# Performance work log

Measured on AMD Instinct MI355X. Metric: run time of the kernel, lower is better.

The kernel has to match this reference:

```python
import jax, jax.numpy as jnp
import numpy as np

K = 16  # hardcoded knn count in Density_loss.forward


def _knn_dist(x, k):
    """Squared pairwise distances [B,N,N], then k smallest per point -> [B,N,k]."""
    sq = jnp.sum(x * x, axis=-1)  # [B,N]
    # d[b,i,j] = |xi|^2 + |xj|^2 - 2 xi.xj
    d = sq[:, :, None] + sq[:, None, :] - 2.0 * jnp.einsum('bic,bjc->bij', x, x)
    neg_topk, _ = jax.lax.top_k(-d, k)  # k smallest distances
    return -neg_topk  # [B,N,k]


def setup_inputs() -> dict:
    key = jax.random.key(0)
    k1, k2 = jax.random.split(key)
    seed = jax.random.normal(k1, (8, 2048, 3), dtype=jnp.float32)
    gt_s = jax.random.normal(k2, (8, 2048, 3), dtype=jnp.float32)
    return {"seed": seed, "gt_s": gt_s}


def reference(seed, gt_s):
    seed_dis = _knn_dist(seed, K).mean(axis=-1)  # [B,N]
    gt_dis = _knn_dist(gt_s, K).mean(axis=-1)    # [B,N]
    # dis_avg=True branch: average over points -> [B], then MSE
    dis = seed_dis.mean(axis=-1)
    gt = gt_dis.mean(axis=-1)
    return jnp.mean((dis - gt) ** 2)
```

## Files before the change

### kernel.cpp

```cpp
#include <hip/hip_runtime.h>
#include <math.h>


#define NPTS 2048
#define KSEL 16
#define WAVES_PER_BLOCK 8
#define BLOCK (WAVES_PER_BLOCK * 64)
#define PTS_PER_BLOCK (WAVES_PER_BLOCK * 2)
#define NGROUPS (NPTS / PTS_PER_BLOCK)
#define NBLOCKS (2 * 8 * NGROUPS)

__device__ __forceinline__ int mbcnt64(unsigned long long m) {
  return __builtin_amdgcn_mbcnt_hi(
      (unsigned)(m >> 32), __builtin_amdgcn_mbcnt_lo((unsigned)m, 0u));
}

template <int CTRL, int ROW_MASK>
__device__ __forceinline__ float dpp_add(float v) {
  const int t = __builtin_amdgcn_update_dpp(0, __float_as_int(v), CTRL,
                                            ROW_MASK, 0xf, true);
  return v + __int_as_float(t);
}

__device__ __forceinline__ float wave_sum_dpp(float v) {
  v = dpp_add<0x111, 0xf>(v);
  v = dpp_add<0x112, 0xf>(v);
  v = dpp_add<0x114, 0xf>(v);
  v = dpp_add<0x118, 0xf>(v);
  v = dpp_add<0x142, 0xa>(v);
  v = dpp_add<0x143, 0xc>(v);
  return __int_as_float(__builtin_amdgcn_readlane(__float_as_int(v), 63));
}

__device__ __forceinline__ float dist2(float px, float py, float pz,
                                       float cx, float cy, float cz) {
  float dx = px - cx, dy = py - cy, dz = pz - cz;
  return fmaf(dz, dz, fmaf(dy, dy, dx * dx));
}

__device__ __forceinline__ void gather_candidates(
    const float (&gm)[8], float thr, float px, float py, float pz, int lane,
    const float* xs, const float* ys, const float* zs, int* scrI, bool& ok,
    float& d0, float& d1, float& d2, float& d3) {
  unsigned qmask = 0u;
  int qg = 0;
  #pragma unroll
  for (int m = 0; m < 8; ++m) {
    const bool q = gm[m] <= thr;
    qmask |= q ? (1u << m) : 0u;
    qg += q ? 1 : 0;
  }
  const unsigned long long b0 = __ballot((qg & 1) != 0);
  const unsigned long long b1 = __ballot((qg & 2) != 0);
  const unsigned long long b2 = __ballot((qg & 4) != 0);
  const unsigned long long b3 = __ballot((qg & 8) != 0);
  const int pre =
      mbcnt64(b0) + 2 * mbcnt64(b1) + 4 * mbcnt64(b2) + 8 * mbcnt64(b3);
  const int tot = __popcll(b0) + 2 * __popcll(b1) + 4 * __popcll(b2) +
                  8 * __popcll(b3);
  ok = (tot <= 64);
  if (ok) {
    int pos = pre;
    unsigned mrem = qmask;
    #pragma unroll
    for (int k = 0; k < 2; ++k) {
      const bool w = (mrem != 0u);
      const int m = __ffs(mrem) - 1;
      if (w) scrI[pos] = (lane << 3) | m;
      pos += w ? 1 : 0;
      mrem = w ? (mrem & (mrem - 1u)) : 0u;
    }
    if (__ballot(mrem != 0u) != 0ull) {
      #pragma unroll
      for (int k = 0; k < 6; ++k) {
        const bool w = (mrem != 0u);
        const int m = __ffs(mrem) - 1;
        if (w) scrI[pos] = (lane << 3) | m;
        pos += w ? 1 : 0;
        mrem = w ? (mrem & (mrem - 1u)) : 0u;
      }
    }
  }
  d0 = INFINITY; d1 = INFINITY; d2 = INFINITY; d3 = INFINITY;
  if (ok && lane < tot) {
    const int id = scrI[lane];
    const int o = ((id >> 3) << 2) + ((id & 7) << 8);
    const float4 cx4 = *(const float4*)&xs[o];
    const float4 cy4 = *(const float4*)&ys[o];
    const float4 cz4 = *(const float4*)&zs[o];
    d0 = dist2(px, py, pz, cx4.x, cy4.x, cz4.x);
    d1 = dist2(px, py, pz, cx4.y, cy4.y, cz4.y);
    d2 = dist2(px, py, pz, cx4.z, cy4.z, cz4.z);
    d3 = dist2(px, py, pz, cx4.w, cy4.w, cz4.w);
  }
}

__device__ float fallback_sum16(float px, float py, float pz, int lane,
                                const float* xs, const float* ys,
                                const float* zs) {
  float s = 0.f;
  unsigned consumed = 0u;
  #pragma unroll 1
  for (int r = 0; r < KSEL; ++r) {
    float bv = INFINITY;
    int bi = 0;
    #pragma unroll
    for (int m = 0; m < 8; ++m) {
      const int o = (lane << 2) + (m << 8);
      const float4 cx4 = *(const float4*)&xs[o];
      const float4 cy4 = *(const float4*)&ys[o];
      const float4 cz4 = *(const float4*)&zs[o];
      float dd;
      bool okb;
      dd = dist2(px, py, pz, cx4.x, cy4.x, cz4.x);
      okb = (((consumed >> ((m << 2) + 0)) & 1u) == 0u) && (dd < bv);
      bv = okb ? dd : bv; bi = okb ? ((m << 2) + 0) : bi;
      dd = dist2(px, py, pz, cx4.y, cy4.y, cz4.y);
      okb = (((consumed >> ((m << 2) + 1)) & 1u) == 0u) && (dd < bv);
      bv = okb ? dd : bv; bi = okb ? ((m << 2) + 1) : bi;
      dd = dist2(px, py, pz, cx4.z, cy4.z, cz4.z);
      okb = (((consumed >> ((m << 2) + 2)) & 1u) == 0u) && (dd < bv);
      bv = okb ? dd : bv; bi = okb ? ((m << 2) + 2) : bi;
      dd = dist2(px, py, pz, cx4.w, cy4.w, cz4.w);
      okb = (((consumed >> ((m << 2) + 3)) & 1u) == 0u) && (dd < bv);
      bv = okb ? dd : bv; bi = okb ? ((m << 2) + 3) : bi;
    }
    int bl = lane;
    #pragma unroll
    for (int ofs = 32; ofs >= 1; ofs >>= 1) {
      float ov = __shfl_xor(bv, ofs);
      int ol = __shfl_xor(bl, ofs);
      bool take = (ov < bv) || (ov == bv && ol < bl);
      bv = take ? ov : bv;
      bl = take ? ol : bl;
    }
    s += bv;
    if (lane == bl) consumed |= (1u << bi);
  }
  return s;
}

__global__ __launch_bounds__(BLOCK) void knn_sum16_kernel(
    const float* __restrict__ seed, const float* __restrict__ gt,
    float* __restrict__ out_part) {
  __shared__ float xs[NPTS];
  __shared__ float ys[NPTS];
  __shared__ float zs[NPTS];
  __shared__ int scrI[WAVES_PER_BLOCK][2][64];
  __shared__ float bsums[WAVES_PER_BLOCK];

  const int bid = blockIdx.x;
  const int t = bid >> 10;
  const int b = (bid >> 7) & 7;
  const int g = bid & 127;
  const float* base = (t == 0 ? seed : gt) + b * NPTS * 3;

  const int tid = threadIdx.x;

  {
    const float4* src = (const float4*)base;
    float4 f0 = src[3 * tid + 0];
    float4 f1 = src[3 * tid + 1];
    float4 f2 = src[3 * tid + 2];
    *(float4*)&xs[4 * tid] = make_float4(f0.x, f0.w, f1.z, f2.y);
    *(float4*)&ys[4 * tid] = make_float4(f0.y, f1.x, f1.w, f2.z);
    *(float4*)&zs[4 * tid] = make_float4(f0.z, f1.y, f2.x, f2.w);
  }
  __syncthreads();

  const int wave = tid >> 6;
  const int lane = tid & 63;
  const int iA = g * PTS_PER_BLOCK + wave * 2;
  const int iB = iA + 1;
  const float pax = xs[iA], pay = ys[iA], paz = zs[iA];
  const float pbx = xs[iB], pby = ys[iB], pbz = zs[iB];

  float gmA[8], gmB[8];
  #pragma unroll
  for (int m = 0; m < 8; ++m) {
    const int o = (lane << 2) + (m << 8);
    const float4 cx4 = *(const float4*)&xs[o];
    const float4 cy4 = *(const float4*)&ys[o];
    const float4 cz4 = *(const float4*)&zs[o];
    float a0 = dist2(pax, pay, paz, cx4.x, cy4.x, cz4.x);
    float a1 = dist2(pax, pay, paz, cx4.y, cy4.y, cz4.y);
    float a2 = dist2(pax, pay, paz, cx4.z, cy4.z, cz4.z);
    float a3 = dist2(pax, pay, paz, cx4.w, cy4.w, cz4.w);
    gmA[m] = fminf(fminf(a0, a1), fminf(a2, a3));
    float b0 = dist2(pbx, pby, pbz, cx4.x, cy4.x, cz4.x);
    float b1 = dist2(pbx, pby, pbz, cx4.y, cy4.y, cz4.y);
    float b2 = dist2(pbx, pby, pbz, cx4.z, cy4.z, cz4.z);
    float b3 = dist2(pbx, pby, pbz, cx4.w, cy4.w, cz4.w);
    gmB[m] = fminf(fminf(b0, b1), fminf(b2, b3));
  }
  float lminA = gmA[0], lminB = gmB[0];
  #pragma unroll
  for (int m = 1; m < 8; ++m) {
    lminA = fminf(lminA, gmA[m]);
    lminB = fminf(lminB, gmB[m]);
  }

  const unsigned uA = __float_as_uint(lminA);
  const unsigned uB = __float_as_uint(lminB);
  unsigned loA = 0u, hiA = 0x7F800000u, loB = 0u, hiB = 0x7F800000u;
  bool thA = false, thB = false;
  #pragma unroll 1
  for (int r = 0; r < 16; ++r) {
    if (thA && thB) break;
    const unsigned midA = (loA + hiA) >> 1;
    const unsigned midB = (loB + hiB) >> 1;
    const int cA = __popcll(__ballot(uA <= midA));
    const int cB = __popcll(__ballot(uB <= midB));
    if (!thA) {
      const bool gA = cA >= KSEL;
      hiA = gA ? midA : hiA;
      loA = gA ? loA : midA;
      thA = (cA >= KSEL) && (cA <= 24);
    }
    if (!thB) {
      const bool gB = cB >= KSEL;
      hiB = gB ? midB : hiB;
      loB = gB ? loB : midB;
      thB = (cB >= KSEL) && (cB <= 24);
    }
  }
  const float thrA = __uint_as_float(hiA);
  const float thrB = __uint_as_float(hiB);

  bool okA, okB;
  float a0, a1, a2, a3, b0, b1, b2, b3;
  gather_candidates(gmA, thrA, pax, pay, paz, lane, xs, ys, zs,
                    &scrI[wave][0][0], okA, a0, a1, a2, a3);
  gather_candidates(gmB, thrB, pbx, pby, pbz, lane, xs, ys, zs,
                    &scrI[wave][1][0], okB, b0, b1, b2, b3);

  const unsigned wa0 = __float_as_uint(a0) + 1u, wa1 = __float_as_uint(a1) + 1u;
  const unsigned wa2 = __float_as_uint(a2) + 1u, wa3 = __float_as_uint(a3) + 1u;
  const unsigned wb0 = __float_as_uint(b0) + 1u, wb1 = __float_as_uint(b1) + 1u;
  const unsigned wb2 = __float_as_uint(b2) + 1u, wb3 = __float_as_uint(b3) + 1u;
  unsigned eloA = 0u, ehiA = 0x7F800001u, eloB = 0u, ehiB = 0x7F800001u;
  bool hA = false, hB = false;
  unsigned sA = 0u, sB = 0u;
  #pragma unroll 1
  for (int r = 0; r < 32; ++r) {
    const bool needA = okA && !hA;
    const bool needB = okB && !hB;
    if (!(needA || needB)) break;
    const unsigned midA = (eloA + ehiA) >> 1;
    const unsigned midB = (eloB + ehiB) >> 1;
    const int cA = __popcll(__ballot(wa0 <= midA)) +
                   __popcll(__ballot(wa1 <= midA)) +
                   __popcll(__ballot(wa2 <= midA)) +
                   __popcll(__ballot(wa3 <= midA));
    const int cB = __popcll(__ballot(wb0 <= midB)) +
                   __popcll(__ballot(wb1 <= midB)) +
                   __popcll(__ballot(wb2 <= midB)) +
                   __popcll(__ballot(wb3 <= midB));
    if (needA) {
      if (cA >= KSEL) ehiA = midA; else eloA = midA;
      if (cA == KSEL) { hA = true; sA = midA; }
    }
    if (needB) {
      if (cB >= KSEL) ehiB = midB; else eloB = midB;
      if (cB == KSEL) { hB = true; sB = midB; }
    }
  }
  float extraA = 0.f, extraB = 0.f;
  if (okA && !hA) {
    sA = eloA;
    const int nlo = __popcll(__ballot(wa0 <= eloA)) +
                    __popcll(__ballot(wa1 <= eloA)) +
                    __popcll(__ballot(wa2 <= eloA)) +
                    __popcll(__ballot(wa3 <= eloA));
    extraA = (float)(KSEL - nlo) * __uint_as_float(ehiA - 1u);
  }
  if (okB && !hB) {
    sB = eloB;
    const int nlo = __popcll(__ballot(wb0 <= eloB)) +
                    __popcll(__ballot(wb1 <= eloB)) +
                    __popcll(__ballot(wb2 <= eloB)) +
                    __popcll(__ballot(wb3 <= eloB));
    extraB = (float)(KSEL - nlo) * __uint_as_float(ehiB - 1u);
  }
  float ca = 0.f, cb = 0.f;
  if (okA) {
    ca = ((wa0 <= sA) ? a0 : 0.f) + ((wa1 <= sA) ? a1 : 0.f) +
         ((wa2 <= sA) ? a2 : 0.f) + ((wa3 <= sA) ? a3 : 0.f);
  }
  if (okB) {
    cb = ((wb0 <= sB) ? b0 : 0.f) + ((wb1 <= sB) ? b1 : 0.f) +
         ((wb2 <= sB) ? b2 : 0.f) + ((wb3 <= sB) ? b3 : 0.f);
  }
  const float caT = wave_sum_dpp(ca);
  const float cbT = wave_sum_dpp(cb);
  float sumA = caT + extraA;
  float sumB = cbT + extraB;
  if (!okA) sumA = fallback_sum16(pax, pay, paz, lane, xs, ys, zs);
  if (!okB) sumB = fallback_sum16(pbx, pby, pbz, lane, xs, ys, zs);

  if (lane == 0) bsums[wave] = sumA + sumB;
  __syncthreads();
  if (tid == 0) {
    float s = 0.f;
    #pragma unroll
    for (int w = 0; w < WAVES_PER_BLOCK; ++w) s += bsums[w];
    out_part[bid] = s;
  }
}

__global__ __launch_bounds__(1024) void final_reduce_kernel(
    const float* __restrict__ parts, float* __restrict__ out) {
  __shared__ float partial[16];
  const int tid = threadIdx.x;
  const int wave = tid >> 6;
  const int lane = tid & 63;
  float s = parts[wave * NGROUPS + lane] + parts[wave * NGROUPS + 64 + lane];
  #pragma unroll
  for (int ofs = 32; ofs >= 1; ofs >>= 1) s += __shfl_xor(s, ofs);
  if (lane == 0) partial[wave] = s;
  __syncthreads();
  if (tid == 0) {
    const float scale = 1.f / (2048.f * 16.f);
    float acc = 0.f;
    #pragma unroll
    for (int bb = 0; bb < 8; ++bb) {
      float diff = (partial[bb] - partial[8 + bb]) * scale;
      acc += diff * diff;
    }
    out[0] = acc * 0.125f;
  }
}

extern "C" void kernel_launch(void* const* d_in, const int* in_sizes, int n_in,
                              void* d_out, int out_size, void* d_ws, size_t ws_size,
                              hipStream_t stream) {
  const float* seed = (const float*)d_in[0];
  const float* gt = (const float*)d_in[1];
  float* out = (float*)d_out;
  float* ws = (float*)d_ws;

  knn_sum16_kernel<<<NBLOCKS, BLOCK, 0, stream>>>(seed, gt, ws);
  final_reduce_kernel<<<1, 1024, 0, stream>>>(ws, out);
}
```

Before: 93.08 us.

## Halve block count with two items per block and seed bisection bounds

Each block now processes two 16-point items, so the shared-memory staging of the point cloud is amortized over twice the work and the grid shrinks from 2048 to 1024 blocks. The first bisection seeds its bounds with fixed float thresholds chosen for unit-normal data. The second bisection starts from the first pass's threshold and a lower bound six exponents below it, and gains an early exit once the interval collapses. This cuts ballot iterations and redundant loads but lowers parallelism, and the fixed seeds assume a particular distance scale.

```diff
diff --git a/kernel.cpp b/kernel.cpp
--- a/kernel.cpp
+++ b/kernel.cpp
@@ -6,9 +6,9 @@
 #define KSEL 16
 #define WAVES_PER_BLOCK 8
 #define BLOCK (WAVES_PER_BLOCK * 64)
-#define PTS_PER_BLOCK (WAVES_PER_BLOCK * 2)
-#define NGROUPS (NPTS / PTS_PER_BLOCK)
-#define NBLOCKS (2 * 8 * NGROUPS)
+#define PTS_PER_ITEM (WAVES_PER_BLOCK * 2)
+#define NITEMS_PER_TB (NPTS / PTS_PER_ITEM)
+#define NBLOCKS (2 * 8 * (NITEMS_PER_TB / 2))
 
 __device__ __forceinline__ int mbcnt64(unsigned long long m) {
   return __builtin_amdgcn_mbcnt_hi(
@@ -140,37 +140,10 @@
   return s;
 }
 
-__global__ __launch_bounds__(BLOCK) void knn_sum16_kernel(
-    const float* __restrict__ seed, const float* __restrict__ gt,
-    float* __restrict__ out_part) {
-  __shared__ float xs[NPTS];
-  __shared__ float ys[NPTS];
-  __shared__ float zs[NPTS];
-  __shared__ int scrI[WAVES_PER_BLOCK][2][64];
-  __shared__ float bsums[WAVES_PER_BLOCK];
-
-  const int bid = blockIdx.x;
-  const int t = bid >> 10;
-  const int b = (bid >> 7) & 7;
-  const int g = bid & 127;
-  const float* base = (t == 0 ? seed : gt) + b * NPTS * 3;
-
-  const int tid = threadIdx.x;
-
-  {
-    const float4* src = (const float4*)base;
-    float4 f0 = src[3 * tid + 0];
-    float4 f1 = src[3 * tid + 1];
-    float4 f2 = src[3 * tid + 2];
-    *(float4*)&xs[4 * tid] = make_float4(f0.x, f0.w, f1.z, f2.y);
-    *(float4*)&ys[4 * tid] = make_float4(f0.y, f1.x, f1.w, f2.z);
-    *(float4*)&zs[4 * tid] = make_float4(f0.z, f1.y, f2.x, f2.w);
-  }
-  __syncthreads();
-
-  const int wave = tid >> 6;
-  const int lane = tid & 63;
-  const int iA = g * PTS_PER_BLOCK + wave * 2;
+__device__ float item_pair_sum(int g, int wave, int lane, const float* xs,
+                               const float* ys, const float* zs, int* scrI0,
+                               int* scrI1) {
+  const int iA = g * PTS_PER_ITEM + wave * 2;
   const int iB = iA + 1;
   const float pax = xs[iA], pay = ys[iA], paz = zs[iA];
   const float pbx = xs[iB], pby = ys[iB], pbz = zs[iB];
@@ -202,8 +175,20 @@
 
   const unsigned uA = __float_as_uint(lminA);
   const unsigned uB = __float_as_uint(lminB);
+  const unsigned SH = 0x3E800000u;
+  const unsigned SL = 0x3B000000u;
   unsigned loA = 0u, hiA = 0x7F800000u, loB = 0u, hiB = 0x7F800000u;
   bool thA = false, thB = false;
+  {
+    const int cA = __popcll(__ballot(uA <= SH));
+    const int cB = __popcll(__ballot(uB <= SH));
+    if (cA >= KSEL) { hiA = SH; thA = (cA <= 24); }
+    if (cB >= KSEL) { hiB = SH; thB = (cB <= 24); }
+    const int dA = __popcll(__ballot(uA <= SL));
+    const int dB = __popcll(__ballot(uB <= SL));
+    if (dA < KSEL) loA = SL;
+    if (dB < KSEL) loB = SL;
+  }
   #pragma unroll 1
   for (int r = 0; r < 16; ++r) {
     if (thA && thB) break;
@@ -229,22 +214,37 @@
 
   bool okA, okB;
   float a0, a1, a2, a3, b0, b1, b2, b3;
-  gather_candidates(gmA, thrA, pax, pay, paz, lane, xs, ys, zs,
-                    &scrI[wave][0][0], okA, a0, a1, a2, a3);
-  gather_candidates(gmB, thrB, pbx, pby, pbz, lane, xs, ys, zs,
-                    &scrI[wave][1][0], okB, b0, b1, b2, b3);
+  gather_candidates(gmA, thrA, pax, pay, paz, lane, xs, ys, zs, scrI0, okA,
+                    a0, a1, a2, a3);
+  gather_candidates(gmB, thrB, pbx, pby, pbz, lane, xs, ys, zs, scrI1, okB,
+                    b0, b1, b2, b3);
 
   const unsigned wa0 = __float_as_uint(a0) + 1u, wa1 = __float_as_uint(a1) + 1u;
   const unsigned wa2 = __float_as_uint(a2) + 1u, wa3 = __float_as_uint(a3) + 1u;
   const unsigned wb0 = __float_as_uint(b0) + 1u, wb1 = __float_as_uint(b1) + 1u;
   const unsigned wb2 = __float_as_uint(b2) + 1u, wb3 = __float_as_uint(b3) + 1u;
-  unsigned eloA = 0u, ehiA = 0x7F800001u, eloB = 0u, ehiB = 0x7F800001u;
+  unsigned eloA = 0u, ehiA = hiA + 1u;
+  unsigned eloB = 0u, ehiB = hiB + 1u;
+  {
+    const unsigned esA = (hiA >= (6u << 23)) ? hiA - (6u << 23) : 0u;
+    const unsigned esB = (hiB >= (6u << 23)) ? hiB - (6u << 23) : 0u;
+    const int nA = __popcll(__ballot(wa0 <= esA)) +
+                   __popcll(__ballot(wa1 <= esA)) +
+                   __popcll(__ballot(wa2 <= esA)) +
+                   __popcll(__ballot(wa3 <= esA));
+    const int nB = __popcll(__ballot(wb0 <= esB)) +
+                   __popcll(__ballot(wb1 <= esB)) +
+                   __popcll(__ballot(wb2 <= esB)) +
+                   __popcll(__ballot(wb3 <= esB));
+    if (nA < KSEL) eloA = esA;
+    if (nB < KSEL) eloB = esB;
+  }
   bool hA = false, hB = false;
   unsigned sA = 0u, sB = 0u;
   #pragma unroll 1
   for (int r = 0; r < 32; ++r) {
-    const bool needA = okA && !hA;
-    const bool needB = okB && !hB;
+    const bool needA = okA && !hA && (ehiA > eloA + 1u);
+    const bool needB = okB && !hB && (ehiB > eloB + 1u);
     if (!(needA || needB)) break;
     const unsigned midA = (eloA + ehiA) >> 1;
     const unsigned midB = (eloB + ehiB) >> 1;
@@ -297,8 +297,46 @@
   float sumB = cbT + extraB;
   if (!okA) sumA = fallback_sum16(pax, pay, paz, lane, xs, ys, zs);
   if (!okB) sumB = fallback_sum16(pbx, pby, pbz, lane, xs, ys, zs);
-
-  if (lane == 0) bsums[wave] = sumA + sumB;
+  return sumA + sumB;
+}
+
+__global__ __launch_bounds__(BLOCK) void knn_sum16_kernel(
+    const float* __restrict__ seed, const float* __restrict__ gt,
+    float* __restrict__ out_part) {
+  __shared__ float xs[NPTS];
+  __shared__ float ys[NPTS];
+  __shared__ float zs[NPTS];
+  __shared__ int scrI[WAVES_PER_BLOCK][2][64];
+  __shared__ float bsums[WAVES_PER_BLOCK];
+
+  const int bid = blockIdx.x;
+  const int t = bid >> 9;
+  const int b = (bid >> 6) & 7;
+  const int j = bid & 63;
+  const float* base = (t == 0 ? seed : gt) + b * NPTS * 3;
+
+  const int tid = threadIdx.x;
+
+  {
+    const float4* src = (const float4*)base;
+    float4 f0 = src[3 * tid + 0];
+    float4 f1 = src[3 * tid + 1];
+    float4 f2 = src[3 * tid + 2];
+    *(float4*)&xs[4 * tid] = make_float4(f0.x, f0.w, f1.z, f2.y);
+    *(float4*)&ys[4 * tid] = make_float4(f0.y, f1.x, f1.w, f2.z);
+    *(float4*)&zs[4 * tid] = make_float4(f0.z, f1.y, f2.x, f2.w);
+  }
+  __syncthreads();
+
+  const int wave = tid >> 6;
+  const int lane = tid & 63;
+
+  float wsum = item_pair_sum(2 * j + 0, wave, lane, xs, ys, zs,
+                             &scrI[wave][0][0], &scrI[wave][1][0]);
+  wsum += item_pair_sum(2 * j + 1, wave, lane, xs, ys, zs,
+                        &scrI[wave][0][0], &scrI[wave][1][0]);
+
+  if (lane == 0) bsums[wave] = wsum;
   __syncthreads();
   if (tid == 0) {
     float s = 0.f;
@@ -314,7 +352,7 @@
   const int tid = threadIdx.x;
   const int wave = tid >> 6;
   const int lane = tid & 63;
-  float s = parts[wave * NGROUPS + lane] + parts[wave * NGROUPS + 64 + lane];
+  float s = parts[wave * 64 + lane];
   #pragma unroll
   for (int ofs = 32; ofs >= 1; ofs >>= 1) s += __shfl_xor(s, ofs);
   if (lane == 0) partial[wave] = s;
```

Result: faster. 90.14 us (median of 2 runs) (-3.2%).
